# Kernel tuning notes

Hardware: AMD Instinct MI355X
Metric: run time of the kernel (lower is better)

Reference implementation:

```python
import jax, jax.numpy as jnp
import numpy as np

H = 50  # hidden_size


def _lstm_layer(x_seq, W_ih, W_hh, b):
    """Single-layer LSTM over a full sequence.
    x_seq: [B, T, D]; W_ih: [4H, D]; W_hh: [4H, H]; b: [4H] (b_ih + b_hh).
    Gate order matches PyTorch: i, f, g, o. Returns hidden seq [B, T, H].
    """
    B = x_seq.shape[0]
    # Precompute the input projection for every timestep in one GEMM.
    xW = jnp.einsum('btd,gd->btg', x_seq, W_ih) + b          # [B, T, 4H]
    xW = jnp.swapaxes(xW, 0, 1)                              # [T, B, 4H] time-major for scan

    def step(carry, xg):
        h, c = carry
        gates = xg + h @ W_hh.T                              # [B, 4H]
        i, f, g, o = jnp.split(gates, 4, axis=-1)
        i = jax.nn.sigmoid(i)
        f = jax.nn.sigmoid(f)
        g = jnp.tanh(g)
        o = jax.nn.sigmoid(o)
        c = f * c + i * g
        h = o * jnp.tanh(c)
        return (h, c), h

    init = (jnp.zeros((B, H), x_seq.dtype), jnp.zeros((B, H), x_seq.dtype))
    _, hs = jax.lax.scan(step, init, xW)                     # hs: [T, B, H]
    return jnp.swapaxes(hs, 0, 1)                            # [B, T, H]


def setup_inputs() -> dict:
    key = jax.random.key(0)
    ks = jax.random.split(key, 9)
    B, T, D, O = 4096, 512, 2, 1
    s = 1.0 / np.sqrt(H)  # PyTorch LSTM init scale: U(-1/sqrt(H), 1/sqrt(H))
    u = lambda k, shape: jax.random.uniform(k, shape, jnp.float32, -s, s)
    return {
        'x': jax.random.normal(ks[0], (B, T, D), jnp.float32),
        'W_ih0': u(ks[1], (4 * H, D)),
        'W_hh0': u(ks[2], (4 * H, H)),
        'b0': u(ks[3], (4 * H,)),   # b_ih + b_hh folded into one bias (identical math)
        'W_ih1': u(ks[4], (4 * H, H)),
        'W_hh1': u(ks[5], (4 * H, H)),
        'b1': u(ks[6], (4 * H,)),
        'W_fc': u(ks[7], (O, H)),
        'b_fc': u(ks[8], (O,)),
    }


def reference(x, W_ih0, W_hh0, b0, W_ih1, W_hh1, b1, W_fc, b_fc):
    h0 = _lstm_layer(x, W_ih0, W_hh0, b0)    # [B, T, H] layer 0
    h1 = _lstm_layer(h0, W_ih1, W_hh1, b1)   # [B, T, H] layer 1
    # Final-step linear head: out = fc(out[:, -1, :])
    return h1[:, -1, :] @ W_fc.T + b_fc      # [B, 1]
```

## Files before the change

kernel.cpp:

```cpp
#include <hip/hip_runtime.h>


typedef _Float16 f16;
typedef f16  f16x8 __attribute__((ext_vector_type(8)));
typedef float f32x4 __attribute__((ext_vector_type(4)));
typedef unsigned short u16;
typedef unsigned int   u32;

#define TT   512
#define MB   16
#define KP   136
#define XTP  513
#define BLK  512

#define EXP2(v) __builtin_amdgcn_exp2f(v)
__device__ __forceinline__ float rcp_(float v) { return __builtin_amdgcn_rcpf(v); }

#define L2E  1.4426950408889634f
#define L2E2 2.8853900817779268f

__device__ __forceinline__ float welem(int layer, int g, int u, int k,
        const float* __restrict__ Whh0,
        const float* __restrict__ Wih1, const float* __restrict__ Whh1) {
    if (u >= 50) return 0.0f;
    const float s = (g == 2) ? L2E2 : -L2E;
    const int row = g * 50 + u;
    if (layer == 0) {
        return (k < 50) ? s * Whh0[row * 50 + k] : 0.0f;
    } else {
        if (k < 50)             return s * Wih1[row * 50 + k];
        if (k >= 64 && k < 114) return s * Whh1[row * 50 + (k - 64)];
        return 0.0f;
    }
}

#define EWFUSED(YI, YF, YG, YO, CS, HOUT)                                     \
    {                                                                         \
        const float eI = EXP2(YI);                                            \
        const float eF = EXP2(YF);                                            \
        const float eG = EXP2(YG);                                            \
        const float eO = EXP2(YO);                                            \
        const float fg  = rcp_(1.0f + eF);                                    \
        const float num = fmaf(L2E2, eG, -L2E2);                              \
        const float igg = num * rcp_((1.0f + eI) * (1.0f + eG));              \
        CS = fmaf(fg, CS, igg);                                               \
        const float cc = fminf(fmaxf(CS, -80.0f), 80.0f);                     \
        const float eC = EXP2(cc);                                            \
        HOUT = (eC - 1.0f) * rcp_((1.0f + eO) * (eC + 1.0f));                 \
    }

extern "C" __global__ void __launch_bounds__(BLK, 2)
lstm2_v8(const float* __restrict__ x,
         const float* __restrict__ W_ih0, const float* __restrict__ W_hh0,
         const float* __restrict__ b0,
         const float* __restrict__ W_ih1, const float* __restrict__ W_hh1,
         const float* __restrict__ b1,
         const float* __restrict__ W_fc,  const float* __restrict__ b_fc,
         float* __restrict__ out)
{
    __shared__ __align__(16) u16 hc[2][MB][KP];
    __shared__ u32   xpack[MB][XTP];
    __shared__ float hfin[MB][52];

    const int tid   = threadIdx.x;
    const int lane  = tid & 63;
    const int wid   = tid >> 6;
    const int layer = wid >> 2;
    const int ub    = wid & 3;
    const int col   = lane & 15;
    const int kg    = lane >> 4;
    const int bbase = blockIdx.x * MB;

    for (int idx = tid; idx < MB * TT; idx += BLK) {
        const int b = idx >> 9, t = idx & (TT - 1);
        const float2 v = *reinterpret_cast<const float2*>(
            x + ((size_t)(bbase + b) * TT + t) * 2);
        xpack[b][t] = (u32)__builtin_bit_cast(u16, (f16)v.x)
                    | ((u32)__builtin_bit_cast(u16, (f16)v.y) << 16);
    }
    {
        u32* hcU = reinterpret_cast<u32*>(&hc[0][0][0]);
        for (int i = tid; i < 2 * MB * KP / 2; i += BLK) hcU[i] = 0;
    }

    const int u = 16 * ub + col;
    f16x8 bf[4][4];
#pragma unroll
    for (int g = 0; g < 4; ++g) {
#pragma unroll
        for (int kf = 0; kf < 4; ++kf) {
            f16x8 v;
#pragma unroll
            for (int e = 0; e < 8; ++e)
                v[e] = (f16)welem(layer, g, u, kf * 32 + 8 * kg + e,
                                  W_hh0, W_ih1, W_hh1);
            bf[g][kf] = v;
        }
    }
    float wxa[4], wxb[4], bsc[4];
    f32x4 biasC[4];
#pragma unroll
    for (int g = 0; g < 4; ++g) {
        const float s = (g == 2) ? L2E2 : -L2E;
        const int row = g * 50 + ((u < 50) ? u : 0);
        const float z50 = (u < 50) ? 1.0f : 0.0f;
        if (layer == 0) {
            wxa[g] = s * W_ih0[row * 2 + 0] * z50;
            wxb[g] = s * W_ih0[row * 2 + 1] * z50;
            bsc[g] = s * b0[row] * z50;
        } else {
            const float bb = s * b1[row] * z50;
            biasC[g] = (f32x4){bb, bb, bb, bb};
            wxa[g] = wxb[g] = bsc[g] = 0.0f;
        }
    }

    float cst[4] = {0.f, 0.f, 0.f, 0.f};
    const f32x4 z = {0.f, 0.f, 0.f, 0.f};
    const int hbase = layer ? 64 : 0;

    __syncthreads();

    f32x4 xc[4];
    if (layer == 0) {
#pragma unroll
        for (int r = 0; r < 4; ++r) {
            const u32 xp = xpack[4 * kg + r][0];
            const float x0 = (float)__builtin_bit_cast(f16, (u16)(xp & 0xffff));
            const float x1 = (float)__builtin_bit_cast(f16, (u16)(xp >> 16));
#pragma unroll
            for (int g = 0; g < 4; ++g)
                xc[g][r] = fmaf(wxa[g], x0, fmaf(wxb[g], x1, bsc[g]));
        }
    }

    for (int it = 0; it <= TT; ++it) {
        const int p = it & 1, q = p ^ 1;
        f32x4 acc[4];

        if (layer == 0) {
            if (it < TT) {
                const f16x8 a0 = *reinterpret_cast<const f16x8*>(&hc[p][col][8 * kg]);
                const f16x8 a1 = *reinterpret_cast<const f16x8*>(&hc[p][col][32 + 8 * kg]);
                __builtin_amdgcn_s_setprio(1);
#pragma unroll
                for (int g = 0; g < 4; ++g) {
                    f32x4 c = __builtin_amdgcn_mfma_f32_16x16x32_f16(a0, bf[g][0], xc[g], 0, 0, 0);
                    acc[g]  = __builtin_amdgcn_mfma_f32_16x16x32_f16(a1, bf[g][1], c, 0, 0, 0);
                }
                __builtin_amdgcn_s_setprio(0);
#pragma unroll
                for (int r = 0; r < 4; ++r) {
                    float hv;
                    EWFUSED(acc[0][r], acc[1][r], acc[2][r], acc[3][r], cst[r], hv);
                    if (u < 50)
                        hc[q][4 * kg + r][u] = __builtin_bit_cast(u16, (f16)hv);
                }
#pragma unroll
                for (int r = 0; r < 4; ++r) {
                    const u32 xp = xpack[4 * kg + r][it + 1];
                    const float x0 = (float)__builtin_bit_cast(f16, (u16)(xp & 0xffff));
                    const float x1 = (float)__builtin_bit_cast(f16, (u16)(xp >> 16));
#pragma unroll
                    for (int g = 0; g < 4; ++g)
                        xc[g][r] = fmaf(wxa[g], x0, fmaf(wxb[g], x1, bsc[g]));
                }
            }
        } else {
            if (it >= 1) {
                const f16x8 a0 = *reinterpret_cast<const f16x8*>(&hc[p][col][8 * kg]);
                const f16x8 a1 = *reinterpret_cast<const f16x8*>(&hc[p][col][32 + 8 * kg]);
                const f16x8 a2 = *reinterpret_cast<const f16x8*>(&hc[p][col][64 + 8 * kg]);
                const f16x8 a3 = *reinterpret_cast<const f16x8*>(&hc[p][col][96 + 8 * kg]);
                __builtin_amdgcn_s_setprio(1);
#pragma unroll
                for (int g = 0; g < 4; ++g) {
                    f32x4 cA = __builtin_amdgcn_mfma_f32_16x16x32_f16(a0, bf[g][0], biasC[g], 0, 0, 0);
                    f32x4 cB = __builtin_amdgcn_mfma_f32_16x16x32_f16(a2, bf[g][2], z, 0, 0, 0);
                    cA = __builtin_amdgcn_mfma_f32_16x16x32_f16(a1, bf[g][1], cA, 0, 0, 0);
                    cB = __builtin_amdgcn_mfma_f32_16x16x32_f16(a3, bf[g][3], cB, 0, 0, 0);
                    acc[g] = cA + cB;
                }
                __builtin_amdgcn_s_setprio(0);
#pragma unroll
                for (int r = 0; r < 4; ++r) {
                    float hv;
                    EWFUSED(acc[0][r], acc[1][r], acc[2][r], acc[3][r], cst[r], hv);
                    if (u < 50) {
                        hc[q][4 * kg + r][64 + u] = __builtin_bit_cast(u16, (f16)hv);
                        if (it == TT) hfin[4 * kg + r][u] = hv;
                    }
                }
            }
        }
        __syncthreads();
    }

    if (tid < MB) {
        float d = b_fc[0];
#pragma unroll
        for (int uu = 0; uu < 50; ++uu) d = fmaf(W_fc[uu], hfin[tid][uu], d);
        out[bbase + tid] = d;
    }
}

extern "C" void kernel_launch(void* const* d_in, const int* in_sizes, int n_in,
                              void* d_out, int out_size, void* d_ws, size_t ws_size,
                              hipStream_t stream) {
    const float* x     = (const float*)d_in[0];
    const float* W_ih0 = (const float*)d_in[1];
    const float* W_hh0 = (const float*)d_in[2];
    const float* b0    = (const float*)d_in[3];
    const float* W_ih1 = (const float*)d_in[4];
    const float* W_hh1 = (const float*)d_in[5];
    const float* b1    = (const float*)d_in[6];
    const float* W_fc  = (const float*)d_in[7];
    const float* b_fc  = (const float*)d_in[8];
    float* out = (float*)d_out;

    const int B = in_sizes[0] / (TT * 2);
    dim3 grid(B / MB), block(BLK);
    hipLaunchKernelGGL(lstm2_v8, grid, block, 0, stream,
                       x, W_ih0, W_hh0, b0, W_ih1, W_hh1, b1, W_fc, b_fc, out);
}
```

Before: 426.3 us.

## Fold input projection and bias into MFMA via augmented K columns

Layer 0's x inputs and a constant 1.0 are written into spare K slots (50-52) of the shared hidden buffer, and the matching W_ih0 and bias values go into the weight fragments. The per-step scalar FMAs for the input projection and bias therefore disappear and the MFMA does that work. Layer 1's bias is folded the same way, and its two parallel accumulation chains become one serial chain of four MFMAs. This trades elementwise VALU work for a longer dependent MFMA chain, and the x and bias values now pass through fp16 precision. The elementwise gate math is also skipped entirely for lanes whose unit index is 50 or above.

```diff
diff --git a/kernel.cpp b/kernel.cpp
--- a/kernel.cpp
+++ b/kernel.cpp
@@ -20,15 +20,21 @@
 #define L2E2 2.8853900817779268f
 
 __device__ __forceinline__ float welem(int layer, int g, int u, int k,
-        const float* __restrict__ Whh0,
-        const float* __restrict__ Wih1, const float* __restrict__ Whh1) {
+        const float* __restrict__ Wih0, const float* __restrict__ Whh0,
+        const float* __restrict__ b0,
+        const float* __restrict__ Wih1, const float* __restrict__ Whh1,
+        const float* __restrict__ b1) {
     if (u >= 50) return 0.0f;
     const float s = (g == 2) ? L2E2 : -L2E;
     const int row = g * 50 + u;
     if (layer == 0) {
-        return (k < 50) ? s * Whh0[row * 50 + k] : 0.0f;
+        if (k < 50)  return s * Whh0[row * 50 + k];
+        if (k < 52)  return s * Wih0[row * 2 + (k - 50)];
+        if (k == 52) return s * b0[row];
+        return 0.0f;
     } else {
         if (k < 50)             return s * Wih1[row * 50 + k];
+        if (k == 52)            return s * b1[row];
         if (k >= 64 && k < 114) return s * Whh1[row * 50 + (k - 64)];
         return 0.0f;
     }
@@ -50,7 +56,7 @@
     }
 
 extern "C" __global__ void __launch_bounds__(BLK, 2)
-lstm2_v8(const float* __restrict__ x,
+lstm2_v9(const float* __restrict__ x,
          const float* __restrict__ W_ih0, const float* __restrict__ W_hh0,
          const float* __restrict__ b0,
          const float* __restrict__ W_ih1, const float* __restrict__ W_hh1,
@@ -82,6 +88,10 @@
         u32* hcU = reinterpret_cast<u32*>(&hc[0][0][0]);
         for (int i = tid; i < 2 * MB * KP / 2; i += BLK) hcU[i] = 0;
     }
+    __syncthreads();
+    if (tid < 32) hc[tid >> 4][tid & 15][52] = (u16)0x3C00;
+    else if (tid < 48)
+        *reinterpret_cast<u32*>(&hc[0][tid - 32][50]) = xpack[tid - 32][0];
 
     const int u = 16 * ub + col;
     f16x8 bf[4][4];
@@ -93,46 +103,14 @@
 #pragma unroll
             for (int e = 0; e < 8; ++e)
                 v[e] = (f16)welem(layer, g, u, kf * 32 + 8 * kg + e,
-                                  W_hh0, W_ih1, W_hh1);
+                                  W_ih0, W_hh0, b0, W_ih1, W_hh1, b1);
             bf[g][kf] = v;
-        }
-    }
-    float wxa[4], wxb[4], bsc[4];
-    f32x4 biasC[4];
-#pragma unroll
-    for (int g = 0; g < 4; ++g) {
-        const float s = (g == 2) ? L2E2 : -L2E;
-        const int row = g * 50 + ((u < 50) ? u : 0);
-        const float z50 = (u < 50) ? 1.0f : 0.0f;
-        if (layer == 0) {
-            wxa[g] = s * W_ih0[row * 2 + 0] * z50;
-            wxb[g] = s * W_ih0[row * 2 + 1] * z50;
-            bsc[g] = s * b0[row] * z50;
-        } else {
-            const float bb = s * b1[row] * z50;
-            biasC[g] = (f32x4){bb, bb, bb, bb};
-            wxa[g] = wxb[g] = bsc[g] = 0.0f;
         }
     }
 
     float cst[4] = {0.f, 0.f, 0.f, 0.f};
     const f32x4 z = {0.f, 0.f, 0.f, 0.f};
-    const int hbase = layer ? 64 : 0;
-
     __syncthreads();
-
-    f32x4 xc[4];
-    if (layer == 0) {
-#pragma unroll
-        for (int r = 0; r < 4; ++r) {
-            const u32 xp = xpack[4 * kg + r][0];
-            const float x0 = (float)__builtin_bit_cast(f16, (u16)(xp & 0xffff));
-            const float x1 = (float)__builtin_bit_cast(f16, (u16)(xp >> 16));
-#pragma unroll
-            for (int g = 0; g < 4; ++g)
-                xc[g][r] = fmaf(wxa[g], x0, fmaf(wxb[g], x1, bsc[g]));
-        }
-    }
 
     for (int it = 0; it <= TT; ++it) {
         const int p = it & 1, q = p ^ 1;
@@ -145,25 +123,17 @@
                 __builtin_amdgcn_s_setprio(1);
 #pragma unroll
                 for (int g = 0; g < 4; ++g) {
-                    f32x4 c = __builtin_amdgcn_mfma_f32_16x16x32_f16(a0, bf[g][0], xc[g], 0, 0, 0);
+                    f32x4 c = __builtin_amdgcn_mfma_f32_16x16x32_f16(a0, bf[g][0], z, 0, 0, 0);
                     acc[g]  = __builtin_amdgcn_mfma_f32_16x16x32_f16(a1, bf[g][1], c, 0, 0, 0);
                 }
                 __builtin_amdgcn_s_setprio(0);
+                if (u < 50) {
 #pragma unroll
-                for (int r = 0; r < 4; ++r) {
-                    float hv;
-                    EWFUSED(acc[0][r], acc[1][r], acc[2][r], acc[3][r], cst[r], hv);
-                    if (u < 50)
+                    for (int r = 0; r < 4; ++r) {
+                        float hv;
+                        EWFUSED(acc[0][r], acc[1][r], acc[2][r], acc[3][r], cst[r], hv);
                         hc[q][4 * kg + r][u] = __builtin_bit_cast(u16, (f16)hv);
-                }
-#pragma unroll
-                for (int r = 0; r < 4; ++r) {
-                    const u32 xp = xpack[4 * kg + r][it + 1];
-                    const float x0 = (float)__builtin_bit_cast(f16, (u16)(xp & 0xffff));
-                    const float x1 = (float)__builtin_bit_cast(f16, (u16)(xp >> 16));
-#pragma unroll
-                    for (int g = 0; g < 4; ++g)
-                        xc[g][r] = fmaf(wxa[g], x0, fmaf(wxb[g], x1, bsc[g]));
+                    }
                 }
             }
         } else {
@@ -175,24 +145,26 @@
                 __builtin_amdgcn_s_setprio(1);
 #pragma unroll
                 for (int g = 0; g < 4; ++g) {
-                    f32x4 cA = __builtin_amdgcn_mfma_f32_16x16x32_f16(a0, bf[g][0], biasC[g], 0, 0, 0);
-                    f32x4 cB = __builtin_amdgcn_mfma_f32_16x16x32_f16(a2, bf[g][2], z, 0, 0, 0);
-                    cA = __builtin_amdgcn_mfma_f32_16x16x32_f16(a1, bf[g][1], cA, 0, 0, 0);
-                    cB = __builtin_amdgcn_mfma_f32_16x16x32_f16(a3, bf[g][3], cB, 0, 0, 0);
-                    acc[g] = cA + cB;
+                    f32x4 c = __builtin_amdgcn_mfma_f32_16x16x32_f16(a0, bf[g][0], z, 0, 0, 0);
+                    c       = __builtin_amdgcn_mfma_f32_16x16x32_f16(a1, bf[g][1], c, 0, 0, 0);
+                    c       = __builtin_amdgcn_mfma_f32_16x16x32_f16(a2, bf[g][2], c, 0, 0, 0);
+                    acc[g]  = __builtin_amdgcn_mfma_f32_16x16x32_f16(a3, bf[g][3], c, 0, 0, 0);
                 }
                 __builtin_amdgcn_s_setprio(0);
+                if (u < 50) {
 #pragma unroll
-                for (int r = 0; r < 4; ++r) {
-                    float hv;
-                    EWFUSED(acc[0][r], acc[1][r], acc[2][r], acc[3][r], cst[r], hv);
-                    if (u < 50) {
+                    for (int r = 0; r < 4; ++r) {
+                        float hv;
+                        EWFUSED(acc[0][r], acc[1][r], acc[2][r], acc[3][r], cst[r], hv);
                         hc[q][4 * kg + r][64 + u] = __builtin_bit_cast(u16, (f16)hv);
                         if (it == TT) hfin[4 * kg + r][u] = hv;
                     }
                 }
             }
         }
+        if (wid == 0 && lane < MB && (it + 1) < TT)
+            *reinterpret_cast<u32*>(&hc[q][lane][50]) = xpack[lane][it + 1];
+
         __syncthreads();
     }
 
@@ -220,6 +192,6 @@
 
     const int B = in_sizes[0] / (TT * 2);
     dim3 grid(B / MB), block(BLK);
-    hipLaunchKernelGGL(lstm2_v8, grid, block, 0, stream,
+    hipLaunchKernelGGL(lstm2_v9, grid, block, 0, stream,
                        x, W_ih0, W_hh0, b0, W_ih1, W_hh1, b1, W_fc, b_fc, out);
 }
```

Result: faster. 373.4 us, median of 2 (-12.4%).
